# Kernel tuning notes

Measured on AMD Instinct MI355X. Metric: run time of the kernel, lower is better.

## Reference

```python
import jax, jax.numpy as jnp
import numpy as np

SEQ_LEN, BATCH, INPUT_DIM, HIDDEN_DIM = 2048, 16, 1024, 2048
COMPRESSION_RATIO = 0.5


def setup_inputs() -> dict:
    key = jax.random.key(0)
    ks = jax.random.split(key, 10)
    s_in = 0.02  # xavier-ish scale for (hidden, input) linears
    return {
        "x": jax.random.normal(ks[0], (SEQ_LEN, BATCH, INPUT_DIM), dtype=jnp.float32),
        "A": jax.random.normal(ks[1], (HIDDEN_DIM, HIDDEN_DIM), dtype=jnp.float32) * 0.1 - 0.5,
        "W_B": jax.random.normal(ks[2], (HIDDEN_DIM, INPUT_DIM), dtype=jnp.float32) * s_in,
        "W_C": jax.random.normal(ks[3], (HIDDEN_DIM, INPUT_DIM), dtype=jnp.float32) * s_in,
        "W_delta": jax.random.normal(ks[4], (HIDDEN_DIM, INPUT_DIM), dtype=jnp.float32) * s_in,
        "b_delta": jnp.zeros((HIDDEN_DIM,), dtype=jnp.float32),
        "W_in": jax.random.normal(ks[5], (HIDDEN_DIM, INPUT_DIM), dtype=jnp.float32) * s_in,
        "b_in": jnp.zeros((HIDDEN_DIM,), dtype=jnp.float32),
        "W_comp": jax.random.normal(ks[6], (INPUT_DIM, HIDDEN_DIM), dtype=jnp.float32) * s_in,
        "b_comp": jnp.zeros((INPUT_DIM,), dtype=jnp.float32),
    }


def reference(x, A, W_B, W_C, W_delta, b_delta, W_in, b_in, W_comp, b_comp):
    # x: (S, B, D_in).  A is an unused parameter in the original forward.
    seq_len = x.shape[0]
    compressed_len = max(1, int(seq_len * COMPRESSION_RATIO))
    step = seq_len // compressed_len

    # Batched projections over all timesteps (replaces per-step Linears)
    B_all = jnp.einsum('sbd,hd->sbh', x, W_B)                       # (S, B, H)
    C_all = jnp.einsum('sbd,hd->sbh', x, W_C)                       # (S, B, H)
    delta = jax.nn.softplus(jnp.einsum('sbd,hd->sbh', x, W_delta) + b_delta)
    u = jnp.einsum('sbd,hd->sbh', x, W_in) + b_in + B_all           # x_proj + B_t

    # Gated linear recurrence: h_t = (1 - delta_t) * h_{t-1} + delta_t * u_t
    def step_fn(h, inp):
        d, uu = inp
        h = (1.0 - d) * h + d * uu
        return h, h

    h0 = jnp.zeros((x.shape[1], u.shape[-1]), dtype=x.dtype)
    _, hs = jax.lax.scan(step_fn, h0, (delta, u))                   # (S, B, H)

    y = C_all * hs                                                  # (S, B, H)

    # Output at the last timestep of each window of size `step`
    idx = np.array([min(i + step, seq_len) - 1 for i in range(0, seq_len, step)])
    y_sel = y[idx]                                                  # (S_c, B, H)
    return jnp.einsum('sbh,dh->sbd', y_sel, W_comp) + b_comp        # (S_c, B, D_in)
```

## Files before the change

kernel.cpp:

```cpp
#include <hip/hip_runtime.h>
#include <hip/hip_bf16.h>
#include <cstdio>

#define S_LEN 2048
#define BATCH 16
#define D_INP 1024
#define H_DIM 2048
#define SC    (S_LEN / 2)
#define BH    (BATCH * H_DIM)
#define NC    16
#define CS    (S_LEN / NC)

typedef __bf16 b16;
typedef __bf16 b16x8 __attribute__((ext_vector_type(8)));
typedef __bf16 b16x4 __attribute__((ext_vector_type(4)));
typedef float  f32x4 __attribute__((ext_vector_type(4)));

__device__ __forceinline__ int sw_off(int r, int k8) {
  return r * 32 + ((k8 ^ ((r >> 1) & 3)) << 3);
}

__device__ __forceinline__ void gl2lds16(const b16* g, b16* l) {
  __builtin_amdgcn_global_load_lds(
      (const __attribute__((address_space(1))) void*)g,
      (__attribute__((address_space(3))) void*)l, 16, 0, 0);
}

__device__ __forceinline__ float softplus_fast(float t) {
  float e = __expf(-fabsf(t));
  return fmaxf(t, 0.f) + __logf(1.f + e);
}

__global__ void cvt_x_kernel(const float* __restrict__ in, b16* __restrict__ out, int n4) {
  int i = blockIdx.x * 256 + threadIdx.x;
  if (i >= n4) return;
  float4 v = ((const float4*)in)[i];
  b16x4 o = {(b16)v.x, (b16)v.y, (b16)v.z, (b16)v.w};
  ((b16x4*)out)[i] = o;
}

__global__ void prep_w_kernel(const float* __restrict__ Wd, const float* __restrict__ Win,
                              const float* __restrict__ WB, const float* __restrict__ Wc,
                              const float* __restrict__ Wcp,
                              b16* __restrict__ Wdu, b16* __restrict__ Wcb,
                              b16* __restrict__ Wcpb) {
  const int HD4 = (H_DIM * D_INP) / 4;
  int i = blockIdx.x * 256 + threadIdx.x;
  if (i >= HD4) return;
  float4 a = ((const float4*)Wd)[i];
  float4 b = ((const float4*)Win)[i];
  float4 c = ((const float4*)WB)[i];
  float4 d = ((const float4*)Wc)[i];
  float4 e = ((const float4*)Wcp)[i];
  ((b16x4*)Wdu)[i] = {(b16)a.x, (b16)a.y, (b16)a.z, (b16)a.w};
  ((b16x4*)Wdu)[HD4 + i] = {(b16)(b.x + c.x), (b16)(b.y + c.y), (b16)(b.z + c.z), (b16)(b.w + c.w)};
  ((b16x4*)Wcb)[i] = {(b16)d.x, (b16)d.y, (b16)d.z, (b16)d.w};
  ((b16x4*)Wcpb)[i] = {(b16)e.x, (b16)e.y, (b16)e.z, (b16)e.w};
}

template <int MODE>
__global__ __launch_bounds__(256, 2) void gemm_bt(
    const b16* __restrict__ A, const b16* __restrict__ W, int K,
    const float* __restrict__ bias0, const float* __restrict__ bias1,
    const b16* __restrict__ hsel, b16* __restrict__ ob0, b16* __restrict__ ob1,
    float* __restrict__ of) {
  __shared__ b16 As[128 * 32];
  __shared__ b16 Bs[128 * 32];
  const int tid  = threadIdx.x;
  const int lane = tid & 63;
  const int wave = tid >> 6;
  const int wr = wave >> 1, wc = wave & 1;
  const int m0 = blockIdx.y * 128;
  const int n0 = blockIdx.x * 128;
  const int lm = lane & 15;
  const int l8 = lane >> 4;
  const int rL  = wave * 16 + (lane >> 2);
  const int k8p = lane & 3;

  f32x4 acc[4][4];
#pragma unroll
  for (int i = 0; i < 4; i++)
#pragma unroll
    for (int j = 0; j < 4; j++) acc[i][j] = (f32x4)0.f;

  for (int k0 = 0; k0 < K; k0 += 32) {
#pragma unroll
    for (int hh = 0; hh < 2; ++hh) {
      const int r = rL + hh * 64;
      const int k8l = k8p ^ ((r >> 1) & 3);
      b16* ldsA = As + (wave * 16 + hh * 64) * 32;
      b16* ldsB = Bs + (wave * 16 + hh * 64) * 32;
      long arow = m0 + r;
      if (MODE == 1) arow = 2 * arow - (arow & 15) + 16;
      gl2lds16(A + arow * (long)K + k0 + k8l * 8, ldsA);
      gl2lds16(W + (long)(n0 + r) * K + k0 + k8l * 8, ldsB);
    }
    __syncthreads();
    b16x8 af[4], bfr[4];
#pragma unroll
    for (int i = 0; i < 4; i++) af[i] = *(const b16x8*)(As + sw_off(wr * 64 + i * 16 + lm, l8));
#pragma unroll
    for (int j = 0; j < 4; j++) bfr[j] = *(const b16x8*)(Bs + sw_off(wc * 64 + j * 16 + lm, l8));
#pragma unroll
    for (int i = 0; i < 4; i++)
#pragma unroll
      for (int j = 0; j < 4; j++)
        acc[i][j] = __builtin_amdgcn_mfma_f32_16x16x32_bf16(af[i], bfr[j], acc[i][j], 0, 0, 0);
    __syncthreads();
  }

  if (MODE == 0) {
    const bool is_delta = (n0 < H_DIM);
    const float* bias = is_delta ? bias0 : bias1;
    b16* ob = is_delta ? ob0 : ob1;
    const int nc0 = (n0 & (H_DIM - 1)) + wc * 64 + lm;
    float bv[4];
#pragma unroll
    for (int j = 0; j < 4; j++) bv[j] = bias[nc0 + j * 16];
#pragma unroll
    for (int i = 0; i < 4; i++) {
      const long rb = m0 + wr * 64 + i * 16 + l8 * 4;
      b16* pr = ob + rb * H_DIM + nc0;
      if (is_delta) {
#pragma unroll
        for (int j = 0; j < 4; j++)
#pragma unroll
          for (int rg = 0; rg < 4; ++rg)
            pr[(long)rg * H_DIM + j * 16] = (b16)softplus_fast(acc[i][j][rg] + bv[j]);
      } else {
#pragma unroll
        for (int j = 0; j < 4; j++)
#pragma unroll
          for (int rg = 0; rg < 4; ++rg)
            pr[(long)rg * H_DIM + j * 16] = (b16)(acc[i][j][rg] + bv[j]);
      }
    }
  } else if (MODE == 1) {
    const int nc0 = n0 + wc * 64 + lm;
#pragma unroll
    for (int i = 0; i < 4; i++) {
      const long rb = m0 + wr * 64 + i * 16 + l8 * 4;
      const b16* hp = hsel + rb * H_DIM + nc0;
      b16* pr = ob0 + rb * H_DIM + nc0;
#pragma unroll
      for (int j = 0; j < 4; j++)
#pragma unroll
        for (int rg = 0; rg < 4; ++rg) {
          float hv = (float)hp[(long)rg * H_DIM + j * 16];
          pr[(long)rg * H_DIM + j * 16] = (b16)(acc[i][j][rg] * hv);
        }
    }
  } else {
    const int nc0 = n0 + wc * 64 + lm;
    float bv[4];
#pragma unroll
    for (int j = 0; j < 4; j++) bv[j] = bias0[nc0 + j * 16];
#pragma unroll
    for (int i = 0; i < 4; i++) {
      const long rb = m0 + wr * 64 + i * 16 + l8 * 4;
      float* pr = of + rb * D_INP + nc0;
#pragma unroll
      for (int j = 0; j < 4; j++)
#pragma unroll
        for (int rg = 0; rg < 4; ++rg)
          pr[(long)rg * D_INP + j * 16] = acc[i][j][rg] + bv[j];
    }
  }
}

__global__ void scan_a_kernel(const b16* __restrict__ dl, const b16* __restrict__ uu,
                              float* __restrict__ P, float* __restrict__ Q) {
  int g = blockIdx.x * 256 + threadIdx.x;
  int c = g >> 15;
  int p = g & (BH - 1);
  const b16* dp = dl + (size_t)c * CS * BH + p;
  const b16* up = uu + (size_t)c * CS * BH + p;
  float h = 0.f, pr = 1.f;
#pragma unroll 4
  for (int s = 0; s < CS; ++s) {
    float d = (float)dp[(size_t)s * BH];
    float u = (float)up[(size_t)s * BH];
    float a = 1.f - d;
    h = a * h + d * u;
    pr *= a;
  }
  P[g] = pr;
  Q[g] = h;
}

__global__ void scan_b_kernel(const float* __restrict__ P, const float* __restrict__ Q,
                              float* __restrict__ Hs) {
  int p = blockIdx.x * 256 + threadIdx.x;
  float h = 0.f;
#pragma unroll
  for (int c = 0; c < NC; ++c) {
    Hs[c * BH + p] = h;
    h = P[c * BH + p] * h + Q[c * BH + p];
  }
}

__global__ void scan_c_kernel(const b16* __restrict__ dl, const b16* __restrict__ uu,
                              const float* __restrict__ Hs, b16* __restrict__ hsel) {
  int g = blockIdx.x * 256 + threadIdx.x;
  int c = g >> 15;
  int p = g & (BH - 1);
  const b16* dp = dl + (size_t)c * CS * BH + p;
  const b16* up = uu + (size_t)c * CS * BH + p;
  b16* hp = hsel + (size_t)(c * (CS / 2)) * BH + p;
  float h = Hs[g];
#pragma unroll 4
  for (int s = 0; s < CS; ++s) {
    float d = (float)dp[(size_t)s * BH];
    float u = (float)up[(size_t)s * BH];
    h = (1.f - d) * h + d * u;
    if (s & 1) hp[(size_t)(s >> 1) * BH] = (b16)h;
  }
}

extern "C" void kernel_launch(void* const* d_in, const int* in_sizes, int n_in,
                              void* d_out, int out_size, void* d_ws, size_t ws_size,
                              hipStream_t stream) {
  const float* x   = (const float*)d_in[0];
  const float* WB  = (const float*)d_in[2];
  const float* Wc  = (const float*)d_in[3];
  const float* Wd  = (const float*)d_in[4];
  const float* bd  = (const float*)d_in[5];
  const float* Win = (const float*)d_in[6];
  const float* bi  = (const float*)d_in[7];
  const float* Wcp = (const float*)d_in[8];
  const float* bc  = (const float*)d_in[9];
  float* out = (float*)d_out;

  char* w = (char*)d_ws;
  size_t off = 0;
  auto alloc = [&](size_t bytes) {
    void* p = w + off;
    off += (bytes + 255) & ~(size_t)255;
    return p;
  };
  b16* xb   = (b16*)alloc((size_t)S_LEN * BATCH * D_INP * 2);
  b16* Wdu  = (b16*)alloc((size_t)2 * H_DIM * D_INP * 2);
  b16* Wcb  = (b16*)alloc((size_t)H_DIM * D_INP * 2);
  b16* Wcpb = (b16*)alloc((size_t)D_INP * H_DIM * 2);
  b16* dbuf = (b16*)alloc((size_t)S_LEN * BH * 2);
  b16* ubuf = (b16*)alloc((size_t)S_LEN * BH * 2);
  b16* hsel = (b16*)alloc((size_t)SC * BH * 2);
  b16* ysel = (b16*)alloc((size_t)SC * BH * 2);
  float* P  = (float*)alloc((size_t)NC * BH * 4);
  float* Q  = (float*)alloc((size_t)NC * BH * 4);
  float* Hs = (float*)alloc((size_t)NC * BH * 4);
  if (off > ws_size) {
    fprintf(stderr, "kernel_launch: ws too small: need %zu have %zu\n", off, ws_size);
    return;
  }

  int n4 = S_LEN * BATCH * D_INP / 4;
  cvt_x_kernel<<<(n4 + 255) / 256, 256, 0, stream>>>(x, xb, n4);
  int hd4 = H_DIM * D_INP / 4;
  prep_w_kernel<<<(hd4 + 255) / 256, 256, 0, stream>>>(Wd, Win, WB, Wc, Wcp, Wdu, Wcb, Wcpb);
  dim3 g1(2 * H_DIM / 128, S_LEN * BATCH / 128);
  gemm_bt<0><<<g1, 256, 0, stream>>>(xb, Wdu, D_INP, bd, bi, nullptr, dbuf, ubuf, nullptr);
  scan_a_kernel<<<NC * BH / 256, 256, 0, stream>>>(dbuf, ubuf, P, Q);
  scan_b_kernel<<<BH / 256, 256, 0, stream>>>(P, Q, Hs);
  scan_c_kernel<<<NC * BH / 256, 256, 0, stream>>>(dbuf, ubuf, Hs, hsel);
  dim3 g2(H_DIM / 128, SC * BATCH / 128);
  gemm_bt<1><<<g2, 256, 0, stream>>>(xb, Wcb, D_INP, nullptr, nullptr, hsel, ysel, nullptr, nullptr);
  dim3 g3(D_INP / 128, SC * BATCH / 128);
  gemm_bt<2><<<g3, 256, 0, stream>>>(ysel, Wcpb, H_DIM, bc, nullptr, nullptr, nullptr, nullptr, out);
}
```

Measured before the change: 881.4 us.

## Add 256x256-tile GEMM with 4-stage LDS pipeline and XCD-aware block swizzle

Adds a gemm256 kernel: 512 threads, 256x256 output tiles, 128KB dynamic LDS holding four stages loaded with async global_load_lds, and a block-index swizzle that groups tiles per XCD. All three GEMMs use it when the larger shared-memory attribute can be set, and fall back to the 128x128 kernel otherwise. The goal is more operand reuse per byte loaded and better hiding of load latency. The costs are fewer workgroups (tail effects on small grids, e.g. the output GEMM has only 256 blocks), heavy register use from 32 accumulators per thread, and low occupancy. The launch_bounds(512,2) hint cannot be met with 128KB of LDS per block.

```diff
diff --git a/kernel.cpp b/kernel.cpp
--- a/kernel.cpp
+++ b/kernel.cpp
@@ -56,6 +56,147 @@
   ((b16x4*)Wdu)[HD4 + i] = {(b16)(b.x + c.x), (b16)(b.y + c.y), (b16)(b.z + c.z), (b16)(b.w + c.w)};
   ((b16x4*)Wcb)[i] = {(b16)d.x, (b16)d.y, (b16)d.z, (b16)d.w};
   ((b16x4*)Wcpb)[i] = {(b16)e.x, (b16)e.y, (b16)e.z, (b16)e.w};
+}
+
+template <int MODE>
+__device__ __forceinline__ void stage256(const b16* __restrict__ A, const b16* __restrict__ W,
+                                         int K, int k0, b16* buf, int m0, int n0,
+                                         int wave, int lane) {
+  const int w = wave & 3;
+  const bool isB = wave >= 4;
+  const int rr = lane >> 2;
+  const int gp = lane & 3;
+#pragma unroll
+  for (int l = 0; l < 4; ++l) {
+    const int rbase = w * 64 + l * 16;
+    const int r = rbase + rr;
+    const int gl = gp ^ ((r >> 1) & 3);
+    b16* dst = buf + (isB ? 256 * 32 : 0) + rbase * 32;
+    const b16* src;
+    if (isB) {
+      src = W + (long)(n0 + r) * K + k0 + gl * 8;
+    } else {
+      long arow = m0 + r;
+      if (MODE == 1) arow = 2 * arow - (arow & 15) + 16;
+      src = A + arow * (long)K + k0 + gl * 8;
+    }
+    gl2lds16(src, dst);
+  }
+}
+
+template <int MODE>
+__global__ __launch_bounds__(512, 2) void gemm256(
+    const b16* __restrict__ A, const b16* __restrict__ W, int K,
+    const float* __restrict__ bias0, const float* __restrict__ bias1,
+    const b16* __restrict__ hsel, b16* __restrict__ ob0, b16* __restrict__ ob1,
+    float* __restrict__ of) {
+  extern __shared__ b16 lds[];
+  const int tid  = threadIdx.x;
+  const int lane = tid & 63;
+  const int wave = tid >> 6;
+  const int wm = wave >> 2, wn = wave & 3;
+  const int lm = lane & 15;
+  const int l8 = lane >> 4;
+
+  const int gx  = gridDim.x;
+  const int nwg = gx * gridDim.y;
+  const int id0 = blockIdx.y * gx + blockIdx.x;
+  const int sw  = (id0 & 7) * (nwg >> 3) + (id0 >> 3);
+  const int m0 = (sw / gx) * 256;
+  const int n0 = (sw % gx) * 256;
+
+  f32x4 acc[8][4];
+#pragma unroll
+  for (int i = 0; i < 8; i++)
+#pragma unroll
+    for (int j = 0; j < 4; j++) acc[i][j] = (f32x4)0.f;
+
+  const int NT = K >> 5;
+  stage256<MODE>(A, W, K, 0,  lds + 0 * 16384, m0, n0, wave, lane);
+  stage256<MODE>(A, W, K, 32, lds + 1 * 16384, m0, n0, wave, lane);
+  stage256<MODE>(A, W, K, 64, lds + 2 * 16384, m0, n0, wave, lane);
+
+  for (int t = 0; t < NT; ++t) {
+    if (t + 2 < NT)      asm volatile("s_waitcnt vmcnt(8)" ::: "memory");
+    else if (t + 1 < NT) asm volatile("s_waitcnt vmcnt(4)" ::: "memory");
+    else                 asm volatile("s_waitcnt vmcnt(0)" ::: "memory");
+    __builtin_amdgcn_s_barrier();
+    if (t + 3 < NT)
+      stage256<MODE>(A, W, K, (t + 3) << 5, lds + (size_t)((t + 3) & 3) * 16384,
+                     m0, n0, wave, lane);
+    const b16* As = lds + (size_t)(t & 3) * 16384;
+    const b16* Bs = As + 256 * 32;
+    b16x8 af[8], bfr[4];
+#pragma unroll
+    for (int i = 0; i < 8; i++) af[i] = *(const b16x8*)(As + sw_off(wm * 128 + i * 16 + lm, l8));
+#pragma unroll
+    for (int j = 0; j < 4; j++) bfr[j] = *(const b16x8*)(Bs + sw_off(wn * 64 + j * 16 + lm, l8));
+    __builtin_amdgcn_s_setprio(1);
+#pragma unroll
+    for (int i = 0; i < 8; i++)
+#pragma unroll
+      for (int j = 0; j < 4; j++)
+        acc[i][j] = __builtin_amdgcn_mfma_f32_16x16x32_bf16(af[i], bfr[j], acc[i][j], 0, 0, 0);
+    __builtin_amdgcn_s_setprio(0);
+  }
+
+  if (MODE == 0) {
+    const bool is_delta = (n0 < H_DIM);
+    const float* bias = is_delta ? bias0 : bias1;
+    b16* ob = is_delta ? ob0 : ob1;
+    const int nc0 = (n0 & (H_DIM - 1)) + wn * 64 + lm;
+    float bv[4];
+#pragma unroll
+    for (int j = 0; j < 4; j++) bv[j] = bias[nc0 + j * 16];
+#pragma unroll
+    for (int i = 0; i < 8; i++) {
+      const long rb = m0 + wm * 128 + i * 16 + l8 * 4;
+      b16* pr = ob + rb * H_DIM + nc0;
+      if (is_delta) {
+#pragma unroll
+        for (int j = 0; j < 4; j++)
+#pragma unroll
+          for (int rg = 0; rg < 4; ++rg)
+            pr[(long)rg * H_DIM + j * 16] = (b16)softplus_fast(acc[i][j][rg] + bv[j]);
+      } else {
+#pragma unroll
+        for (int j = 0; j < 4; j++)
+#pragma unroll
+          for (int rg = 0; rg < 4; ++rg)
+            pr[(long)rg * H_DIM + j * 16] = (b16)(acc[i][j][rg] + bv[j]);
+      }
+    }
+  } else if (MODE == 1) {
+    const int nc0 = n0 + wn * 64 + lm;
+#pragma unroll
+    for (int i = 0; i < 8; i++) {
+      const long rb = m0 + wm * 128 + i * 16 + l8 * 4;
+      const b16* hp = hsel + rb * H_DIM + nc0;
+      b16* pr = ob0 + rb * H_DIM + nc0;
+#pragma unroll
+      for (int j = 0; j < 4; j++)
+#pragma unroll
+        for (int rg = 0; rg < 4; ++rg) {
+          float hv = (float)hp[(long)rg * H_DIM + j * 16];
+          pr[(long)rg * H_DIM + j * 16] = (b16)(acc[i][j][rg] * hv);
+        }
+    }
+  } else {
+    const int nc0 = n0 + wn * 64 + lm;
+    float bv[4];
+#pragma unroll
+    for (int j = 0; j < 4; j++) bv[j] = bias0[nc0 + j * 16];
+#pragma unroll
+    for (int i = 0; i < 8; i++) {
+      const long rb = m0 + wm * 128 + i * 16 + l8 * 4;
+      float* pr = of + rb * D_INP + nc0;
+#pragma unroll
+      for (int j = 0; j < 4; j++)
+#pragma unroll
+        for (int rg = 0; rg < 4; ++rg)
+          pr[(long)rg * D_INP + j * 16] = acc[i][j][rg] + bv[j];
+    }
+  }
 }
 
 template <int MODE>
@@ -254,17 +395,43 @@
     return;
   }
 
+  static int g_big = -1;
+  if (g_big < 0) {
+    hipError_t e0 = hipFuncSetAttribute(reinterpret_cast<const void*>(&gemm256<0>),
+                                        hipFuncAttributeMaxDynamicSharedMemorySize, 131072);
+    hipError_t e1 = hipFuncSetAttribute(reinterpret_cast<const void*>(&gemm256<1>),
+                                        hipFuncAttributeMaxDynamicSharedMemorySize, 131072);
+    hipError_t e2 = hipFuncSetAttribute(reinterpret_cast<const void*>(&gemm256<2>),
+                                        hipFuncAttributeMaxDynamicSharedMemorySize, 131072);
+    g_big = (e0 == hipSuccess && e1 == hipSuccess && e2 == hipSuccess) ? 1 : 0;
+  }
+
   int n4 = S_LEN * BATCH * D_INP / 4;
   cvt_x_kernel<<<(n4 + 255) / 256, 256, 0, stream>>>(x, xb, n4);
   int hd4 = H_DIM * D_INP / 4;
   prep_w_kernel<<<(hd4 + 255) / 256, 256, 0, stream>>>(Wd, Win, WB, Wc, Wcp, Wdu, Wcb, Wcpb);
-  dim3 g1(2 * H_DIM / 128, S_LEN * BATCH / 128);
-  gemm_bt<0><<<g1, 256, 0, stream>>>(xb, Wdu, D_INP, bd, bi, nullptr, dbuf, ubuf, nullptr);
+  if (g_big) {
+    dim3 g1(2 * H_DIM / 256, S_LEN * BATCH / 256);
+    gemm256<0><<<g1, 512, 131072, stream>>>(xb, Wdu, D_INP, bd, bi, nullptr, dbuf, ubuf, nullptr);
+  } else {
+    dim3 g1(2 * H_DIM / 128, S_LEN * BATCH / 128);
+    gemm_bt<0><<<g1, 256, 0, stream>>>(xb, Wdu, D_INP, bd, bi, nullptr, dbuf, ubuf, nullptr);
+  }
   scan_a_kernel<<<NC * BH / 256, 256, 0, stream>>>(dbuf, ubuf, P, Q);
   scan_b_kernel<<<BH / 256, 256, 0, stream>>>(P, Q, Hs);
   scan_c_kernel<<<NC * BH / 256, 256, 0, stream>>>(dbuf, ubuf, Hs, hsel);
-  dim3 g2(H_DIM / 128, SC * BATCH / 128);
-  gemm_bt<1><<<g2, 256, 0, stream>>>(xb, Wcb, D_INP, nullptr, nullptr, hsel, ysel, nullptr, nullptr);
-  dim3 g3(D_INP / 128, SC * BATCH / 128);
-  gemm_bt<2><<<g3, 256, 0, stream>>>(ysel, Wcpb, H_DIM, bc, nullptr, nullptr, nullptr, nullptr, out);
-}
+  if (g_big) {
+    dim3 g2(H_DIM / 256, SC * BATCH / 256);
+    gemm256<1><<<g2, 512, 131072, stream>>>(xb, Wcb, D_INP, nullptr, nullptr, hsel, ysel, nullptr, nullptr);
+  } else {
+    dim3 g2(H_DIM / 128, SC * BATCH / 128);
+    gemm_bt<1><<<g2, 256, 0, stream>>>(xb, Wcb, D_INP, nullptr, nullptr, hsel, ysel, nullptr, nullptr);
+  }
+  if (g_big) {
+    dim3 g3(D_INP / 256, SC * BATCH / 256);
+    gemm256<2><<<g3, 512, 131072, stream>>>(ysel, Wcpb, H_DIM, bc, nullptr, nullptr, nullptr, nullptr, out);
+  } else {
+    dim3 g3(D_INP / 128, SC * BATCH / 128);
+    gemm_bt<2><<<g3, 256, 0, stream>>>(ysel, Wcpb, H_DIM, bc, nullptr, nullptr, nullptr, nullptr, out);
+  }
+}
```

Result: faster. 841.1 us (-4.6%).
